# Performance work log

Measured on AMD Instinct MI355X. Metric: run time of the kernel, lower is better.

## Reference

```python
import jax, jax.numpy as jnp
import numpy as np

D_MODEL = 1024
NUM_HEADS = 16
HEAD_DIM = D_MODEL // NUM_HEADS
D_FF = 4096
B, S = 4, 2048
EPS = 1e-5


def layernorm(x, gamma, beta):
    mu = jnp.mean(x, axis=-1, keepdims=True)
    var = jnp.mean(jnp.square(x - mu), axis=-1, keepdims=True)
    return (x - mu) * jax.lax.rsqrt(var + EPS) * gamma + beta


def setup_inputs() -> dict:
    key = jax.random.key(0)
    ks = jax.random.split(key, 16)
    s_in = 1.0 / np.sqrt(D_MODEL)
    s_ff = 1.0 / np.sqrt(D_FF)
    return {
        "x": jax.random.normal(ks[0], (B, S, D_MODEL), jnp.float32),
        "Wq": jax.random.normal(ks[1], (D_MODEL, D_MODEL), jnp.float32) * s_in,
        "bq": jnp.zeros((D_MODEL,), jnp.float32),
        "Wk": jax.random.normal(ks[2], (D_MODEL, D_MODEL), jnp.float32) * s_in,
        "bk": jnp.zeros((D_MODEL,), jnp.float32),
        "Wv": jax.random.normal(ks[3], (D_MODEL, D_MODEL), jnp.float32) * s_in,
        "bv": jnp.zeros((D_MODEL,), jnp.float32),
        "Wo": jax.random.normal(ks[4], (D_MODEL, D_MODEL), jnp.float32) * s_in,
        "bo": jnp.zeros((D_MODEL,), jnp.float32),
        "W1": jax.random.normal(ks[5], (D_MODEL, D_FF), jnp.float32) * s_in,
        "b1": jnp.zeros((D_FF,), jnp.float32),
        "W2": jax.random.normal(ks[6], (D_FF, D_MODEL), jnp.float32) * s_ff,
        "b2": jnp.zeros((D_MODEL,), jnp.float32),
        "g1": jnp.ones((D_MODEL,), jnp.float32),
        "be1": jnp.zeros((D_MODEL,), jnp.float32),
        "g2": jnp.ones((D_MODEL,), jnp.float32),
        "be2": jnp.zeros((D_MODEL,), jnp.float32),
    }


def reference(x, Wq, bq, Wk, bk, Wv, bv, Wo, bo, W1, b1, W2, b2, g1, be1, g2, be2):
    # multi-head self-attention (dropout is identity at eval)
    def split_heads(t):  # [B,S,D] -> [B,H,S,hd]
        return t.reshape(B, S, NUM_HEADS, HEAD_DIM).transpose(0, 2, 1, 3)

    q = split_heads(x @ Wq + bq)
    k = split_heads(x @ Wk + bk)
    v = split_heads(x @ Wv + bv)
    scores = jnp.einsum("bhqd,bhkd->bhqk", q, k) / np.sqrt(HEAD_DIM)
    attn = jax.nn.softmax(scores, axis=-1)
    out = jnp.einsum("bhqk,bhkd->bhqd", attn, v)
    out = out.transpose(0, 2, 1, 3).reshape(B, S, D_MODEL)
    attn_out = out @ Wo + bo

    h = layernorm(x + attn_out, g1, be1)
    ff = jax.nn.relu(h @ W1 + b1) @ W2 + b2
    return layernorm(h + ff, g2, be2)
```

## Files before the change

kernel.cpp:

```cpp
#include <hip/hip_runtime.h>
#include <hip/hip_bf16.h>


#define DM    1024
#define DFF   4096
#define NH    16
#define HD    64
#define BATCH 4
#define SEQ   2048
#define TOK   (BATCH * SEQ)

typedef __attribute__((ext_vector_type(8))) __bf16 bf16x8;
typedef __attribute__((ext_vector_type(4))) float f32x4;
typedef __attribute__((ext_vector_type(16))) float f32x16;
typedef __attribute__((ext_vector_type(4))) unsigned short u16x4;

typedef const __attribute__((address_space(1))) unsigned int* gas1_t;
typedef __attribute__((address_space(3))) unsigned int* las3_t;

__device__ __forceinline__ void gl_lds16(const void* g, void* l) {
  __builtin_amdgcn_global_load_lds((gas1_t)g, (las3_t)l, 16, 0, 0);
}

__device__ __forceinline__ unsigned short f2bu(float x) {
  return __builtin_bit_cast(unsigned short, __float2bfloat16(x));
}

__device__ __forceinline__ unsigned pk_bf16_trunc(float hi, float lo) {
  return __builtin_amdgcn_perm(__builtin_bit_cast(unsigned, hi),
                               __builtin_bit_cast(unsigned, lo), 0x07060302u);
}

__global__ __launch_bounds__(256) void cast_bf16(
    const float* __restrict__ in, unsigned short* __restrict__ out, int n4) {
  int i = blockIdx.x * 256 + threadIdx.x;
  if (i >= n4) return;
  float4 v = ((const float4*)in)[i];
  u16x4 o = {f2bu(v.x), f2bu(v.y), f2bu(v.z), f2bu(v.w)};
  ((u16x4*)out)[i] = o;
}

__global__ __launch_bounds__(256) void transpose_cast(
    const float* __restrict__ in, unsigned short* __restrict__ out, int K, int N) {
  __shared__ float tile[32][33];
  int n0 = blockIdx.x * 32, k0 = blockIdx.y * 32;
  int tx = threadIdx.x, ty = threadIdx.y;
#pragma unroll
  for (int i = 0; i < 4; ++i)
    tile[ty + 8 * i][tx] = in[(size_t)(k0 + ty + 8 * i) * N + n0 + tx];
  __syncthreads();
#pragma unroll
  for (int i = 0; i < 4; ++i)
    out[(size_t)(n0 + ty + 8 * i) * K + k0 + tx] = f2bu(tile[tx][ty + 8 * i]);
}

__global__ __launch_bounds__(256) void transpose_cast4(
    const float* __restrict__ A0, const float* __restrict__ A1,
    const float* __restrict__ A2, const float* __restrict__ A3,
    unsigned short* __restrict__ O0, unsigned short* __restrict__ O1,
    unsigned short* __restrict__ O2, unsigned short* __restrict__ O3) {
  __shared__ float tile[32][33];
  const float* in; unsigned short* out;
  switch (blockIdx.z) {
    case 0: in = A0; out = O0; break;
    case 1: in = A1; out = O1; break;
    case 2: in = A2; out = O2; break;
    default: in = A3; out = O3; break;
  }
  int n0 = blockIdx.x * 32, k0 = blockIdx.y * 32;
  int tx = threadIdx.x, ty = threadIdx.y;
#pragma unroll
  for (int i = 0; i < 4; ++i)
    tile[ty + 8 * i][tx] = in[(size_t)(k0 + ty + 8 * i) * DM + n0 + tx];
  __syncthreads();
#pragma unroll
  for (int i = 0; i < 4; ++i)
    out[(size_t)(n0 + ty + 8 * i) * DM + k0 + tx] = f2bu(tile[tx][ty + 8 * i]);
}

__device__ __forceinline__ void gemm_mainloop(
    const unsigned short* __restrict__ A, const unsigned short* __restrict__ Bt,
    int K, int m0, int n0, unsigned short* As, unsigned short* Bs,
    f32x16 acc[2][2]) {
  const int tid = threadIdx.x, lane = tid & 63, w = tid >> 6;
  const int l31 = lane & 31, khalf = lane >> 5;
  const int wr = w >> 1, wc = w & 1;
  const int rk = (l31 >> 1) & 3;

  const unsigned short* ag[2];
  const unsigned short* bg[2];
  char* ldsA[2]; char* ldsB[2];
#pragma unroll
  for (int i = 0; i < 2; ++i) {
    int f = (i * 4 + w) * 64 + lane;
    int row = f >> 2;
    int col = ((f & 3) ^ ((row >> 1) & 3)) * 8;
    ag[i] = A + (size_t)(m0 + row) * K + col;
    bg[i] = Bt + (size_t)(n0 + row) * K + col;
    ldsA[i] = (char*)As + (size_t)((i * 4 + w) * 1024);
    ldsB[i] = (char*)Bs + (size_t)((i * 4 + w) * 1024);
  }

  for (int kb = 0; kb < K; kb += 32) {
#pragma unroll
    for (int i = 0; i < 2; ++i) {
      gl_lds16(ag[i], ldsA[i]);
      gl_lds16(bg[i], ldsB[i]);
      ag[i] += 32;
      bg[i] += 32;
    }
    __syncthreads();
#pragma unroll
    for (int kk = 0; kk < 2; ++kk) {
      const int sw = ((kk * 2 + khalf) ^ rk) * 16;
      bf16x8 aF[2], bF[2];
#pragma unroll
      for (int t = 0; t < 2; ++t) {
        aF[t] = *(const bf16x8*)((const char*)As + (wr * 64 + t * 32 + l31) * 64 + sw);
        bF[t] = *(const bf16x8*)((const char*)Bs + (wc * 64 + t * 32 + l31) * 64 + sw);
      }
#pragma unroll
      for (int mi = 0; mi < 2; ++mi)
#pragma unroll
        for (int ni = 0; ni < 2; ++ni)
          acc[mi][ni] = __builtin_amdgcn_mfma_f32_32x32x16_bf16(
              aF[mi], bF[ni], acc[mi][ni], 0, 0, 0);
    }
    __syncthreads();
  }
}


__global__ __launch_bounds__(256) void gemm_bt(
    const unsigned short* __restrict__ A, const unsigned short* __restrict__ Bt,
    const float* __restrict__ bias, void* __restrict__ Cout,
    int N, int K, float alpha, int relu, int ofp32) {
  __shared__ unsigned short As[128 * 32];
  __shared__ unsigned short Bs[128 * 32];
  const int tid = threadIdx.x, lane = tid & 63, w = tid >> 6;
  const int l31 = lane & 31, khalf = lane >> 5;
  const int m0 = blockIdx.y * 128, n0 = blockIdx.x * 128;
  const int wr = w >> 1, wc = w & 1;

  f32x16 acc[2][2];
#pragma unroll
  for (int mi = 0; mi < 2; ++mi)
#pragma unroll
    for (int ni = 0; ni < 2; ++ni)
#pragma unroll
      for (int r = 0; r < 16; ++r) acc[mi][ni][r] = 0.f;

  gemm_mainloop(A, Bt, K, m0, n0, As, Bs, acc);

#pragma unroll
  for (int ni = 0; ni < 2; ++ni) {
    int col = n0 + wc * 64 + ni * 32 + l31;
    float bvv = bias[col];
#pragma unroll
    for (int mi = 0; mi < 2; ++mi) {
#pragma unroll
      for (int g = 0; g < 4; ++g) {
        int rbase = m0 + wr * 64 + mi * 32 + g * 8 + khalf * 4;
#pragma unroll
        for (int r = 0; r < 4; ++r) {
          float val = alpha * (acc[mi][ni][g * 4 + r] + bvv);
          if (relu) val = fmaxf(val, 0.f);
          size_t idx = (size_t)(rbase + r) * N + col;
          if (ofp32) ((float*)Cout)[idx] = val;
          else ((unsigned short*)Cout)[idx] = f2bu(val);
        }
      }
    }
  }
}

#define QSCALE 0.18033688f

__global__ __launch_bounds__(256) void gemm_qkv(
    const unsigned short* __restrict__ A, const unsigned short* __restrict__ Bt,
    const float* __restrict__ bq, const float* __restrict__ bk,
    const float* __restrict__ bv,
    unsigned short* __restrict__ Qb, unsigned short* __restrict__ Kb,
    unsigned short* __restrict__ Vtg) {
  __shared__ unsigned short As[128 * 32];
  __shared__ unsigned short Bs[128 * 32];
  const int tid = threadIdx.x, lane = tid & 63, w = tid >> 6;
  const int l31 = lane & 31, khalf = lane >> 5;
  const int m0 = blockIdx.y * 128, n0 = blockIdx.x * 128;
  const int wr = w >> 1, wc = w & 1;

  f32x16 acc[2][2];
#pragma unroll
  for (int mi = 0; mi < 2; ++mi)
#pragma unroll
    for (int ni = 0; ni < 2; ++ni)
#pragma unroll
      for (int r = 0; r < 16; ++r) acc[mi][ni][r] = 0.f;

  gemm_mainloop(A, Bt, DM, m0, n0, As, Bs, acc);

  const int region = n0 >> 10;
  const int nloc0 = (n0 & 1023) + wc * 64;
  if (region < 2) {
    unsigned short* Out = region ? Kb : Qb;
    const float* bias = region ? bk : bq;
    const float alpha = region ? 1.0f : QSCALE;
#pragma unroll
    for (int ni = 0; ni < 2; ++ni) {
      int col = nloc0 + ni * 32 + l31;
      float bvv = bias[col];
#pragma unroll
      for (int mi = 0; mi < 2; ++mi) {
#pragma unroll
        for (int g = 0; g < 4; ++g) {
          int rbase = m0 + wr * 64 + mi * 32 + g * 8 + khalf * 4;
#pragma unroll
          for (int r = 0; r < 4; ++r)
            Out[(size_t)(rbase + r) * DM + col] =
                f2bu(alpha * (acc[mi][ni][g * 4 + r] + bvv));
        }
      }
    }
  } else {
#pragma unroll
    for (int ni = 0; ni < 2; ++ni) {
      int col = nloc0 + ni * 32 + l31;
      float bvv = bv[col];
      int hh = col >> 6, dl = col & 63;
#pragma unroll
      for (int mi = 0; mi < 2; ++mi) {
#pragma unroll
        for (int g = 0; g < 4; ++g) {
          int sbase = m0 + wr * 64 + mi * 32 + g * 8 + khalf * 4;
          int b_ = sbase >> 11, s0 = sbase & 2047;
          u16x4 pk;
#pragma unroll
          for (int r = 0; r < 4; ++r) pk[r] = f2bu(acc[mi][ni][g * 4 + r] + bvv);
          *(u16x4*)(Vtg + ((size_t)((b_ * NH + hh) * HD + dl)) * SEQ + s0) = pk;
        }
      }
    }
  }
}

__global__ __launch_bounds__(256) void attn_kernel(
    const unsigned short* __restrict__ Q, const unsigned short* __restrict__ K,
    const unsigned short* __restrict__ Vtg, unsigned short* __restrict__ O) {
  __shared__ unsigned short Kt[2][64 * 64];
  __shared__ unsigned short Vt[2][64 * 64];
  __shared__ unsigned short Pt[4][32 * 64];
  __shared__ __align__(16) float redL[4][32];

  const int tid = threadIdx.x, lane = tid & 63, w = tid >> 6;
  const int l15 = lane & 15, quad = lane >> 4;
  const int q0 = blockIdx.x * 128;
  const int bh = blockIdx.y, b = bh >> 4, hh = bh & 15;
  const size_t tokbase = (size_t)b * SEQ;

  bf16x8 qf[2][2];
#pragma unroll
  for (int qg = 0; qg < 2; ++qg)
#pragma unroll
    for (int kk = 0; kk < 2; ++kk)
      qf[qg][kk] = *(const bf16x8*)(Q +
          (tokbase + q0 + w * 32 + qg * 16 + l15) * DM + hh * HD + kk * 32 + quad * 8);

  float l_run[2] = {0.f, 0.f};
  f32x4 Oacc[2][4];
#pragma unroll
  for (int qg = 0; qg < 2; ++qg)
#pragma unroll
    for (int nt = 0; nt < 4; ++nt) Oacc[qg][nt] = {0.f, 0.f, 0.f, 0.f};

  char* ptw = (char*)&Pt[w][0];

  int rowS[2], csrcS[2];
#pragma unroll
  for (int i = 0; i < 2; ++i) {
    int f = (i * 4 + w) * 64 + lane;
    rowS[i] = f >> 3;
    csrcS[i] = ((f & 7) ^ (rowS[i] & 7)) * 8;
  }
  const unsigned short* kg[2];
  const unsigned short* vg[2];
  char* ldsK[2][2]; char* ldsV[2][2];
#pragma unroll
  for (int i = 0; i < 2; ++i) {
    kg[i] = K + (tokbase + rowS[i]) * DM + hh * HD + csrcS[i];
    vg[i] = Vtg + ((size_t)bh * HD + rowS[i]) * SEQ + csrcS[i];
#pragma unroll
    for (int bb = 0; bb < 2; ++bb) {
      ldsK[bb][i] = (char*)Kt[bb] + (size_t)((i * 4 + w) * 1024);
      ldsV[bb][i] = (char*)Vt[bb] + (size_t)((i * 4 + w) * 1024);
    }
  }

#pragma unroll
  for (int i = 0; i < 2; ++i) {
    gl_lds16(kg[i], ldsK[0][i]);
    gl_lds16(vg[i], ldsV[0][i]);
    kg[i] += 64 * DM;
    vg[i] += 64;
  }

  for (int j = 0; j < SEQ / 64; ++j) {
    const int buf = j & 1;
    __syncthreads();
    if (j + 1 < SEQ / 64) {
#pragma unroll
      for (int i = 0; i < 2; ++i) {
        gl_lds16(kg[i], ldsK[buf ^ 1][i]);
        gl_lds16(vg[i], ldsV[buf ^ 1][i]);
        kg[i] += 64 * DM;
        vg[i] += 64;
      }
    }

    const char* ktb = (const char*)Kt[buf];
    const char* vtb = (const char*)Vt[buf];

    f32x4 S[2][4];
#pragma unroll
    for (int qg = 0; qg < 2; ++qg)
#pragma unroll
      for (int mt = 0; mt < 4; ++mt) S[qg][mt] = {0.f, 0.f, 0.f, 0.f};
#pragma unroll
    for (int kk = 0; kk < 2; ++kk) {
#pragma unroll
      for (int mt = 0; mt < 4; ++mt) {
        bf16x8 aK = *(const bf16x8*)(ktb + (mt * 16 + l15) * 128 +
                                     (((kk * 4 + quad) ^ (l15 & 7)) * 16));
        S[0][mt] = __builtin_amdgcn_mfma_f32_16x16x32_bf16(aK, qf[0][kk], S[0][mt], 0, 0, 0);
        S[1][mt] = __builtin_amdgcn_mfma_f32_16x16x32_bf16(aK, qf[1][kk], S[1][mt], 0, 0, 0);
      }
    }

#pragma unroll
    for (int qg = 0; qg < 2; ++qg) {
      float rs = 0.f;
#pragma unroll
      for (int mt = 0; mt < 4; ++mt) {
        float p0 = __builtin_amdgcn_exp2f(S[qg][mt][0]);
        float p1 = __builtin_amdgcn_exp2f(S[qg][mt][1]);
        float p2 = __builtin_amdgcn_exp2f(S[qg][mt][2]);
        float p3 = __builtin_amdgcn_exp2f(S[qg][mt][3]);
        rs += (p0 + p1) + (p2 + p3);
        uint2 pk = {pk_bf16_trunc(p1, p0), pk_bf16_trunc(p3, p2)};
        *(uint2*)(ptw + (qg * 16 + l15) * 128 +
                  (((mt * 2 + (quad >> 1)) ^ (l15 & 7)) * 16 + (quad & 1) * 8)) = pk;
      }
      l_run[qg] += rs;
    }

#pragma unroll
    for (int kk = 0; kk < 2; ++kk) {
      bf16x8 aP[2];
#pragma unroll
      for (int qg = 0; qg < 2; ++qg)
        aP[qg] = *(const bf16x8*)(ptw + (qg * 16 + l15) * 128 +
                                  (((kk * 4 + quad) ^ (l15 & 7)) * 16));
#pragma unroll
      for (int nt = 0; nt < 4; ++nt) {
        bf16x8 bV = *(const bf16x8*)(vtb + (nt * 16 + l15) * 128 +
                                     (((kk * 4 + quad) ^ (l15 & 7)) * 16));
        Oacc[0][nt] = __builtin_amdgcn_mfma_f32_16x16x32_bf16(aP[0], bV, Oacc[0][nt], 0, 0, 0);
        Oacc[1][nt] = __builtin_amdgcn_mfma_f32_16x16x32_bf16(aP[1], bV, Oacc[1][nt], 0, 0, 0);
      }
    }
  }

#pragma unroll
  for (int qg = 0; qg < 2; ++qg) {
    l_run[qg] += __shfl_xor(l_run[qg], 16);
    l_run[qg] += __shfl_xor(l_run[qg], 32);
    if (lane < 16) redL[w][qg * 16 + l15] = l_run[qg];
  }
#pragma unroll
  for (int qg = 0; qg < 2; ++qg) {
    f32x4 lv = *(const f32x4*)&redL[w][qg * 16 + quad * 4];
    f32x4 li;
#pragma unroll
    for (int r = 0; r < 4; ++r) li[r] = 1.0f / lv[r];
#pragma unroll
    for (int nt = 0; nt < 4; ++nt)
#pragma unroll
      for (int r = 0; r < 4; ++r) {
        size_t tok = tokbase + q0 + w * 32 + qg * 16 + quad * 4 + r;
        O[tok * DM + hh * HD + nt * 16 + l15] = f2bu(Oacc[qg][nt][r] * li[r]);
      }
  }
}

__global__ __launch_bounds__(256) void ln_res(
    const float* __restrict__ base, const float* __restrict__ delta,
    const float* __restrict__ gamma, const float* __restrict__ beta,
    float* __restrict__ outf, unsigned short* __restrict__ outb) {
  __shared__ float red[8];
  const int row = blockIdx.x, tid = threadIdx.x;
  const size_t rb = (size_t)row * DM;
  float4 xv = ((const float4*)(base + rb))[tid];
  float4 dv = ((const float4*)(delta + rb))[tid];
  float s0 = xv.x + dv.x, s1 = xv.y + dv.y, s2 = xv.z + dv.z, s3 = xv.w + dv.w;
  float t = s0 + s1 + s2 + s3;
#pragma unroll
  for (int m = 1; m < 64; m <<= 1) t += __shfl_xor(t, m);
  if ((tid & 63) == 0) red[tid >> 6] = t;
  __syncthreads();
  float mu = (red[0] + red[1] + red[2] + red[3]) * (1.0f / DM);
  float d0 = s0 - mu, d1 = s1 - mu, d2 = s2 - mu, d3 = s3 - mu;
  float v = d0 * d0 + d1 * d1 + d2 * d2 + d3 * d3;
#pragma unroll
  for (int m = 1; m < 64; m <<= 1) v += __shfl_xor(v, m);
  if ((tid & 63) == 0) red[4 + (tid >> 6)] = v;
  __syncthreads();
  float var = (red[4] + red[5] + red[6] + red[7]) * (1.0f / DM);
  float rs = rsqrtf(var + 1e-5f);
  float4 gv = ((const float4*)gamma)[tid];
  float4 bv = ((const float4*)beta)[tid];
  float o0 = d0 * rs * gv.x + bv.x;
  float o1 = d1 * rs * gv.y + bv.y;
  float o2 = d2 * rs * gv.z + bv.z;
  float o3 = d3 * rs * gv.w + bv.w;
  float4 ov = {o0, o1, o2, o3};
  ((float4*)(outf + rb))[tid] = ov;
  if (outb) {
    u16x4 ob = {f2bu(o0), f2bu(o1), f2bu(o2), f2bu(o3)};
    ((u16x4*)(outb + rb))[tid] = ob;
  }
}

extern "C" void kernel_launch(void* const* d_in, const int* in_sizes, int n_in,
                              void* d_out, int out_size, void* d_ws, size_t ws_size,
                              hipStream_t stream) {
  const float* x   = (const float*)d_in[0];
  const float* Wq  = (const float*)d_in[1];  const float* bq  = (const float*)d_in[2];
  const float* Wk  = (const float*)d_in[3];  const float* bk  = (const float*)d_in[4];
  const float* Wv  = (const float*)d_in[5];  const float* bvv = (const float*)d_in[6];
  const float* Wo  = (const float*)d_in[7];  const float* bo  = (const float*)d_in[8];
  const float* W1  = (const float*)d_in[9];  const float* b1  = (const float*)d_in[10];
  const float* W2  = (const float*)d_in[11]; const float* b2  = (const float*)d_in[12];
  const float* g1  = (const float*)d_in[13]; const float* be1 = (const float*)d_in[14];
  const float* g2  = (const float*)d_in[15]; const float* be2 = (const float*)d_in[16];

  char* ws = (char*)d_ws;
  const size_t MB = 1ull << 20;
  unsigned short* xb    = (unsigned short*)(ws + 0 * MB);
  unsigned short* wqkvT = (unsigned short*)(ws + 16 * MB);
  unsigned short* woT   = (unsigned short*)(ws + 22 * MB);
  unsigned short* w1T   = (unsigned short*)(ws + 24 * MB);
  unsigned short* w2T   = (unsigned short*)(ws + 32 * MB);
  unsigned short* Qb    = (unsigned short*)(ws + 40 * MB);
  unsigned short* Kb    = (unsigned short*)(ws + 56 * MB);
  unsigned short* Vtg   = (unsigned short*)(ws + 72 * MB);
  unsigned short* aO    = (unsigned short*)(ws + 104 * MB);
  float*          prj   = (float*)(ws + 120 * MB);
  float*          h     = (float*)(ws + 152 * MB);
  unsigned short* hb    = (unsigned short*)(ws + 0 * MB);
  unsigned short* ffm   = (unsigned short*)(ws + 40 * MB);
  float*          ffo   = (float*)(ws + 104 * MB);
  (void)ws_size; (void)in_sizes; (void)n_in; (void)out_size;

  cast_bf16<<<TOK * DM / 4 / 256, 256, 0, stream>>>(x, xb, TOK * DM / 4);
  transpose_cast4<<<dim3(DM / 32, DM / 32, 4), dim3(32, 8), 0, stream>>>(
      Wq, Wk, Wv, Wo, wqkvT, wqkvT + 1024 * 1024, wqkvT + 2048 * 1024, woT);
  transpose_cast<<<dim3(DFF / 32, DM / 32), dim3(32, 8), 0, stream>>>(W1, w1T, DM, DFF);
  transpose_cast<<<dim3(DM / 32, DFF / 32), dim3(32, 8), 0, stream>>>(W2, w2T, DFF, DM);

  gemm_qkv<<<dim3(3 * DM / 128, TOK / 128), 256, 0, stream>>>(
      xb, wqkvT, bq, bk, bvv, Qb, Kb, Vtg);

  attn_kernel<<<dim3(SEQ / 128, BATCH * NH), 256, 0, stream>>>(Qb, Kb, Vtg, aO);

  gemm_bt<<<dim3(DM / 128, TOK / 128), 256, 0, stream>>>(aO, woT, bo, prj, DM, DM, 1.0f, 0, 1);
  ln_res<<<TOK, 256, 0, stream>>>(x, prj, g1, be1, h, hb);

  gemm_bt<<<dim3(DFF / 128, TOK / 128), 256, 0, stream>>>(hb, w1T, b1, ffm, DFF, DM, 1.0f, 1, 0);
  gemm_bt<<<dim3(DM / 128, TOK / 128), 256, 0, stream>>>(ffm, w2T, b2, ffo, DM, DFF, 1.0f, 0, 1);

  ln_res<<<TOK, 256, 0, stream>>>(h, ffo, g2, be2, (float*)d_out, nullptr);
}
```

Baseline: 604.2 us.

## Switch GEMMs to 256x256 tiles with double-buffered pipelined mainloop and split-K FFN2

Replaces the 128x128 single-buffer GEMM mainloop with a 256x256-tile, 512-thread kernel. It uses K=64 double-buffered LDS staging, issues loads in quarters interleaved with MFMA phases via explicit vmcnt waits and barriers, and raises MFMA priority with setprio. The FFN down-projection is split into two K halves written to separate fp32 buffers, and the final layernorm sums both partials. This aims to raise arithmetic intensity and overlap global loads with compute, at the cost of more LDS and registers per block and fewer blocks for the 1024-wide GEMMs.

```diff
diff --git a/kernel.cpp b/kernel.cpp
--- a/kernel.cpp
+++ b/kernel.cpp
@@ -78,167 +78,222 @@
     out[(size_t)(n0 + ty + 8 * i) * DM + k0 + tx] = f2bu(tile[tx][ty + 8 * i]);
 }
 
-__device__ __forceinline__ void gemm_mainloop(
-    const unsigned short* __restrict__ A, const unsigned short* __restrict__ Bt,
-    int K, int m0, int n0, unsigned short* As, unsigned short* Bs,
-    f32x16 acc[2][2]) {
+template <int QM, int QN>
+__device__ __forceinline__ void phase_mma(
+    const unsigned short* As, const unsigned short* Bs, int bufofs,
+    int wr, int wc, int l31, int khalf, f32x16 acc[2][2][2]) {
+  const char* Ah = (const char*)(As + bufofs + QM * 8192);
+  const char* Bh = (const char*)(Bs + bufofs + QN * 8192);
+  const int rA0 = wr * 64 + l31, rA1 = rA0 + 32, rB = wc * 32 + l31;
+  bf16x8 a0[4], a1[4], bb[4];
+#pragma unroll
+  for (int ks = 0; ks < 4; ++ks) {
+    const int c = ks * 2 + khalf;
+    a0[ks] = *(const bf16x8*)(Ah + rA0 * 128 + ((c ^ (rA0 & 7)) << 4));
+    a1[ks] = *(const bf16x8*)(Ah + rA1 * 128 + ((c ^ (rA1 & 7)) << 4));
+    bb[ks] = *(const bf16x8*)(Bh + rB * 128 + ((c ^ (rB & 7)) << 4));
+  }
+  __builtin_amdgcn_s_setprio(1);
+#pragma unroll
+  for (int ks = 0; ks < 4; ++ks) {
+    acc[QM][QN][0] = __builtin_amdgcn_mfma_f32_32x32x16_bf16(
+        a0[ks], bb[ks], acc[QM][QN][0], 0, 0, 0);
+    acc[QM][QN][1] = __builtin_amdgcn_mfma_f32_32x32x16_bf16(
+        a1[ks], bb[ks], acc[QM][QN][1], 0, 0, 0);
+  }
+  __builtin_amdgcn_s_setprio(0);
+}
+
+__device__ __forceinline__ void mainloop256(
+    const unsigned short* __restrict__ A, int lda,
+    const unsigned short* __restrict__ Bt, int ldb, int Kl,
+    int m0, int n0, unsigned short* As, unsigned short* Bs,
+    f32x16 acc[2][2][2]) {
   const int tid = threadIdx.x, lane = tid & 63, w = tid >> 6;
   const int l31 = lane & 31, khalf = lane >> 5;
-  const int wr = w >> 1, wc = w & 1;
-  const int rk = (l31 >> 1) & 3;
-
-  const unsigned short* ag[2];
-  const unsigned short* bg[2];
-  char* ldsA[2]; char* ldsB[2];
-#pragma unroll
-  for (int i = 0; i < 2; ++i) {
-    int f = (i * 4 + w) * 64 + lane;
-    int row = f >> 2;
-    int col = ((f & 3) ^ ((row >> 1) & 3)) * 8;
-    ag[i] = A + (size_t)(m0 + row) * K + col;
-    bg[i] = Bt + (size_t)(n0 + row) * K + col;
-    ldsA[i] = (char*)As + (size_t)((i * 4 + w) * 1024);
-    ldsB[i] = (char*)Bs + (size_t)((i * 4 + w) * 1024);
-  }
-
-  for (int kb = 0; kb < K; kb += 32) {
+  const int wr = w >> 2, wc = w & 3;
+
+  const unsigned short* pa[2][2];
+  const unsigned short* pb[2][2];
+#pragma unroll
+  for (int h = 0; h < 2; ++h)
 #pragma unroll
     for (int i = 0; i < 2; ++i) {
-      gl_lds16(ag[i], ldsA[i]);
-      gl_lds16(bg[i], ldsB[i]);
-      ag[i] += 32;
-      bg[i] += 32;
-    }
-    __syncthreads();
-#pragma unroll
-    for (int kk = 0; kk < 2; ++kk) {
-      const int sw = ((kk * 2 + khalf) ^ rk) * 16;
-      bf16x8 aF[2], bF[2];
-#pragma unroll
-      for (int t = 0; t < 2; ++t) {
-        aF[t] = *(const bf16x8*)((const char*)As + (wr * 64 + t * 32 + l31) * 64 + sw);
-        bF[t] = *(const bf16x8*)((const char*)Bs + (wc * 64 + t * 32 + l31) * 64 + sw);
-      }
-#pragma unroll
-      for (int mi = 0; mi < 2; ++mi)
-#pragma unroll
-        for (int ni = 0; ni < 2; ++ni)
-          acc[mi][ni] = __builtin_amdgcn_mfma_f32_32x32x16_bf16(
-              aF[mi], bF[ni], acc[mi][ni], 0, 0, 0);
-    }
-    __syncthreads();
-  }
-}
-
-
-__global__ __launch_bounds__(256) void gemm_bt(
-    const unsigned short* __restrict__ A, const unsigned short* __restrict__ Bt,
-    const float* __restrict__ bias, void* __restrict__ Cout,
-    int N, int K, float alpha, int relu, int ofp32) {
-  __shared__ unsigned short As[128 * 32];
-  __shared__ unsigned short Bs[128 * 32];
+      const int g = (i * 8 + w) * 64 + lane;
+      const int r = g >> 3;
+      const int cs = ((g & 7) ^ (r & 7)) * 8;
+      pa[h][i] = A + (size_t)(m0 + h * 128 + r) * lda + cs;
+      pb[h][i] = Bt + (size_t)(n0 + h * 128 + r) * ldb + cs;
+    }
+  const int wofs = w * 512;
+
+#define STA(BUF, H, I) gl_lds16(pa[H][I], As + (BUF) * 16384 + (H) * 8192 + (I) * 4096 + wofs)
+#define STB(BUF, H, I) gl_lds16(pb[H][I], Bs + (BUF) * 16384 + (H) * 8192 + (I) * 4096 + wofs)
+#define ADV_A(H) { pa[H][0] += 64; pa[H][1] += 64; }
+#define ADV_B(H) { pb[H][0] += 64; pb[H][1] += 64; }
+
+  STA(0, 0, 0); STA(0, 0, 1); ADV_A(0);
+  STB(0, 0, 0); STB(0, 0, 1); ADV_B(0);
+  STB(0, 1, 0); STB(0, 1, 1); ADV_B(1);
+  STA(0, 1, 0); STA(0, 1, 1); ADV_A(1);
+
+#define PH(BUF, QMv, QNv, WAITSTR, STG)                                  \
+  asm volatile(WAITSTR ::: "memory");                                    \
+  STG;                                                                   \
+  phase_mma<QMv, QNv>(As, Bs, (BUF) * 16384, wr, wc, l31, khalf, acc)
+
+#define TILE_STEADY(B)                                                        \
+  PH(B, 0, 0, "s_waitcnt vmcnt(4)\n\ts_barrier",                              \
+     { STA(B ^ 1, 0, 0); STA(B ^ 1, 0, 1); ADV_A(0); });                      \
+  PH(B, 0, 1, "s_waitcnt vmcnt(4)\n\ts_barrier",                              \
+     { STB(B ^ 1, 0, 0); STB(B ^ 1, 0, 1); ADV_B(0); });                      \
+  PH(B, 1, 0, "s_waitcnt vmcnt(4)\n\ts_barrier",                              \
+     { STB(B ^ 1, 1, 0); STB(B ^ 1, 1, 1); ADV_B(1); });                      \
+  PH(B, 1, 1, "s_barrier",                                                    \
+     { STA(B ^ 1, 1, 0); STA(B ^ 1, 1, 1); ADV_A(1); })
+
+  const int NT = Kl >> 6;
+  for (int t = 0; t + 2 < NT; t += 2) {
+    TILE_STEADY(0);
+    TILE_STEADY(1);
+  }
+  TILE_STEADY(0);
+  PH(1, 0, 0, "s_waitcnt vmcnt(4)\n\ts_barrier", {});
+  PH(1, 0, 1, "s_waitcnt vmcnt(2)\n\ts_barrier", {});
+  PH(1, 1, 0, "s_waitcnt vmcnt(0)\n\ts_barrier", {});
+  PH(1, 1, 1, "s_barrier", {});
+
+#undef TILE_STEADY
+#undef PH
+#undef ADV_B
+#undef ADV_A
+#undef STB
+#undef STA
+}
+
+
+__global__ __launch_bounds__(512, 2) void gemm256(
+    const unsigned short* __restrict__ A, int lda,
+    const unsigned short* __restrict__ Bt, int ldb, int Kl,
+    const float* __restrict__ bias, void* __restrict__ C0,
+    void* __restrict__ C1, int N, float alpha, int relu, int ofp32) {
+  __shared__ unsigned short As[32768];
+  __shared__ unsigned short Bs[32768];
   const int tid = threadIdx.x, lane = tid & 63, w = tid >> 6;
   const int l31 = lane & 31, khalf = lane >> 5;
-  const int m0 = blockIdx.y * 128, n0 = blockIdx.x * 128;
-  const int wr = w >> 1, wc = w & 1;
-
-  f32x16 acc[2][2];
-#pragma unroll
-  for (int mi = 0; mi < 2; ++mi)
-#pragma unroll
-    for (int ni = 0; ni < 2; ++ni)
-#pragma unroll
-      for (int r = 0; r < 16; ++r) acc[mi][ni][r] = 0.f;
-
-  gemm_mainloop(A, Bt, K, m0, n0, As, Bs, acc);
-
-#pragma unroll
-  for (int ni = 0; ni < 2; ++ni) {
-    int col = n0 + wc * 64 + ni * 32 + l31;
-    float bvv = bias[col];
-#pragma unroll
-    for (int mi = 0; mi < 2; ++mi) {
-#pragma unroll
-      for (int g = 0; g < 4; ++g) {
-        int rbase = m0 + wr * 64 + mi * 32 + g * 8 + khalf * 4;
-#pragma unroll
-        for (int r = 0; r < 4; ++r) {
-          float val = alpha * (acc[mi][ni][g * 4 + r] + bvv);
-          if (relu) val = fmaxf(val, 0.f);
-          size_t idx = (size_t)(rbase + r) * N + col;
-          if (ofp32) ((float*)Cout)[idx] = val;
-          else ((unsigned short*)Cout)[idx] = f2bu(val);
+  const int wr = w >> 2, wc = w & 3;
+  const int m0 = blockIdx.y * 256, n0 = blockIdx.x * 256;
+  const int koff = blockIdx.z * Kl;
+  void* Cout = blockIdx.z ? C1 : C0;
+  const float* be = blockIdx.z ? nullptr : bias;
+
+  f32x16 acc[2][2][2];
+#pragma unroll
+  for (int qm = 0; qm < 2; ++qm)
+#pragma unroll
+    for (int qn = 0; qn < 2; ++qn)
+#pragma unroll
+      for (int mi = 0; mi < 2; ++mi)
+#pragma unroll
+        for (int r = 0; r < 16; ++r) acc[qm][qn][mi][r] = 0.f;
+
+  mainloop256(A + koff, lda, Bt + koff, ldb, Kl, m0, n0, As, Bs, acc);
+
+#pragma unroll
+  for (int qn = 0; qn < 2; ++qn) {
+    const int col = n0 + qn * 128 + wc * 32 + l31;
+    const float bvv = be ? be[col] : 0.f;
+#pragma unroll
+    for (int qm = 0; qm < 2; ++qm)
+#pragma unroll
+      for (int mi = 0; mi < 2; ++mi) {
+#pragma unroll
+        for (int g = 0; g < 4; ++g) {
+          const int rbase = m0 + qm * 128 + wr * 64 + mi * 32 + g * 8 + khalf * 4;
+#pragma unroll
+          for (int r = 0; r < 4; ++r) {
+            float val = alpha * (acc[qm][qn][mi][g * 4 + r] + bvv);
+            if (relu) val = fmaxf(val, 0.f);
+            size_t idx = (size_t)(rbase + r) * N + col;
+            if (ofp32) ((float*)Cout)[idx] = val;
+            else ((unsigned short*)Cout)[idx] = f2bu(val);
+          }
         }
       }
-    }
   }
 }
 
 #define QSCALE 0.18033688f
 
-__global__ __launch_bounds__(256) void gemm_qkv(
+__global__ __launch_bounds__(512, 2) void gemm_qkv256(
     const unsigned short* __restrict__ A, const unsigned short* __restrict__ Bt,
     const float* __restrict__ bq, const float* __restrict__ bk,
     const float* __restrict__ bv,
     unsigned short* __restrict__ Qb, unsigned short* __restrict__ Kb,
     unsigned short* __restrict__ Vtg) {
-  __shared__ unsigned short As[128 * 32];
-  __shared__ unsigned short Bs[128 * 32];
+  __shared__ unsigned short As[32768];
+  __shared__ unsigned short Bs[32768];
   const int tid = threadIdx.x, lane = tid & 63, w = tid >> 6;
   const int l31 = lane & 31, khalf = lane >> 5;
-  const int m0 = blockIdx.y * 128, n0 = blockIdx.x * 128;
-  const int wr = w >> 1, wc = w & 1;
-
-  f32x16 acc[2][2];
-#pragma unroll
-  for (int mi = 0; mi < 2; ++mi)
-#pragma unroll
-    for (int ni = 0; ni < 2; ++ni)
-#pragma unroll
-      for (int r = 0; r < 16; ++r) acc[mi][ni][r] = 0.f;
-
-  gemm_mainloop(A, Bt, DM, m0, n0, As, Bs, acc);
+  const int wr = w >> 2, wc = w & 3;
+  const int m0 = blockIdx.y * 256, n0 = blockIdx.x * 256;
+
+  f32x16 acc[2][2][2];
+#pragma unroll
+  for (int qm = 0; qm < 2; ++qm)
+#pragma unroll
+    for (int qn = 0; qn < 2; ++qn)
+#pragma unroll
+      for (int mi = 0; mi < 2; ++mi)
+#pragma unroll
+        for (int r = 0; r < 16; ++r) acc[qm][qn][mi][r] = 0.f;
+
+  mainloop256(A, DM, Bt, DM, DM, m0, n0, As, Bs, acc);
 
   const int region = n0 >> 10;
-  const int nloc0 = (n0 & 1023) + wc * 64;
   if (region < 2) {
     unsigned short* Out = region ? Kb : Qb;
     const float* bias = region ? bk : bq;
     const float alpha = region ? 1.0f : QSCALE;
 #pragma unroll
-    for (int ni = 0; ni < 2; ++ni) {
-      int col = nloc0 + ni * 32 + l31;
-      float bvv = bias[col];
-#pragma unroll
-      for (int mi = 0; mi < 2; ++mi) {
-#pragma unroll
-        for (int g = 0; g < 4; ++g) {
-          int rbase = m0 + wr * 64 + mi * 32 + g * 8 + khalf * 4;
-#pragma unroll
-          for (int r = 0; r < 4; ++r)
-            Out[(size_t)(rbase + r) * DM + col] =
-                f2bu(alpha * (acc[mi][ni][g * 4 + r] + bvv));
+    for (int qn = 0; qn < 2; ++qn) {
+      const int col = (n0 & 1023) + qn * 128 + wc * 32 + l31;
+      const float bvv = bias[col];
+#pragma unroll
+      for (int qm = 0; qm < 2; ++qm)
+#pragma unroll
+        for (int mi = 0; mi < 2; ++mi) {
+#pragma unroll
+          for (int g = 0; g < 4; ++g) {
+            const int rbase = m0 + qm * 128 + wr * 64 + mi * 32 + g * 8 + khalf * 4;
+#pragma unroll
+            for (int r = 0; r < 4; ++r)
+              Out[(size_t)(rbase + r) * DM + col] =
+                  f2bu(alpha * (acc[qm][qn][mi][g * 4 + r] + bvv));
+          }
         }
-      }
     }
   } else {
 #pragma unroll
-    for (int ni = 0; ni < 2; ++ni) {
-      int col = nloc0 + ni * 32 + l31;
-      float bvv = bv[col];
-      int hh = col >> 6, dl = col & 63;
-#pragma unroll
-      for (int mi = 0; mi < 2; ++mi) {
-#pragma unroll
-        for (int g = 0; g < 4; ++g) {
-          int sbase = m0 + wr * 64 + mi * 32 + g * 8 + khalf * 4;
-          int b_ = sbase >> 11, s0 = sbase & 2047;
-          u16x4 pk;
-#pragma unroll
-          for (int r = 0; r < 4; ++r) pk[r] = f2bu(acc[mi][ni][g * 4 + r] + bvv);
-          *(u16x4*)(Vtg + ((size_t)((b_ * NH + hh) * HD + dl)) * SEQ + s0) = pk;
+    for (int qn = 0; qn < 2; ++qn) {
+      const int col = (n0 & 1023) + qn * 128 + wc * 32 + l31;
+      const float bvv = bv[col];
+      const int hh = col >> 6, dl = col & 63;
+#pragma unroll
+      for (int qm = 0; qm < 2; ++qm)
+#pragma unroll
+        for (int mi = 0; mi < 2; ++mi) {
+#pragma unroll
+          for (int g = 0; g < 4; ++g) {
+            const int sbase = m0 + qm * 128 + wr * 64 + mi * 32 + g * 8 + khalf * 4;
+            const int b_ = sbase >> 11, s0 = sbase & 2047;
+            u16x4 pk;
+#pragma unroll
+            for (int r = 0; r < 4; ++r)
+              pk[r] = f2bu(acc[qm][qn][mi][g * 4 + r] + bvv);
+            *(u16x4*)(Vtg + ((size_t)((b_ * NH + hh) * HD + dl)) * SEQ + s0) = pk;
+          }
         }
-      }
     }
   }
 }
@@ -392,23 +447,28 @@
 }
 
 __global__ __launch_bounds__(256) void ln_res(
-    const float* __restrict__ base, const float* __restrict__ delta,
+    const float* __restrict__ base, const float* __restrict__ d0,
+    const float* __restrict__ d1,
     const float* __restrict__ gamma, const float* __restrict__ beta,
     float* __restrict__ outf, unsigned short* __restrict__ outb) {
   __shared__ float red[8];
   const int row = blockIdx.x, tid = threadIdx.x;
   const size_t rb = (size_t)row * DM;
   float4 xv = ((const float4*)(base + rb))[tid];
-  float4 dv = ((const float4*)(delta + rb))[tid];
+  float4 dv = ((const float4*)(d0 + rb))[tid];
   float s0 = xv.x + dv.x, s1 = xv.y + dv.y, s2 = xv.z + dv.z, s3 = xv.w + dv.w;
+  if (d1) {
+    float4 ev = ((const float4*)(d1 + rb))[tid];
+    s0 += ev.x; s1 += ev.y; s2 += ev.z; s3 += ev.w;
+  }
   float t = s0 + s1 + s2 + s3;
 #pragma unroll
   for (int m = 1; m < 64; m <<= 1) t += __shfl_xor(t, m);
   if ((tid & 63) == 0) red[tid >> 6] = t;
   __syncthreads();
   float mu = (red[0] + red[1] + red[2] + red[3]) * (1.0f / DM);
-  float d0 = s0 - mu, d1 = s1 - mu, d2 = s2 - mu, d3 = s3 - mu;
-  float v = d0 * d0 + d1 * d1 + d2 * d2 + d3 * d3;
+  float dd0 = s0 - mu, dd1 = s1 - mu, dd2 = s2 - mu, dd3 = s3 - mu;
+  float v = dd0 * dd0 + dd1 * dd1 + dd2 * dd2 + dd3 * dd3;
 #pragma unroll
   for (int m = 1; m < 64; m <<= 1) v += __shfl_xor(v, m);
   if ((tid & 63) == 0) red[4 + (tid >> 6)] = v;
@@ -417,10 +477,10 @@
   float rs = rsqrtf(var + 1e-5f);
   float4 gv = ((const float4*)gamma)[tid];
   float4 bv = ((const float4*)beta)[tid];
-  float o0 = d0 * rs * gv.x + bv.x;
-  float o1 = d1 * rs * gv.y + bv.y;
-  float o2 = d2 * rs * gv.z + bv.z;
-  float o3 = d3 * rs * gv.w + bv.w;
+  float o0 = dd0 * rs * gv.x + bv.x;
+  float o1 = dd1 * rs * gv.y + bv.y;
+  float o2 = dd2 * rs * gv.z + bv.z;
+  float o3 = dd3 * rs * gv.w + bv.w;
   float4 ov = {o0, o1, o2, o3};
   ((float4*)(outf + rb))[tid] = ov;
   if (outb) {
@@ -458,6 +518,7 @@
   unsigned short* hb    = (unsigned short*)(ws + 0 * MB);
   unsigned short* ffm   = (unsigned short*)(ws + 40 * MB);
   float*          ffo   = (float*)(ws + 104 * MB);
+  float*          ffo2  = (float*)(ws + 0 * MB);
   (void)ws_size; (void)in_sizes; (void)n_in; (void)out_size;
 
   cast_bf16<<<TOK * DM / 4 / 256, 256, 0, stream>>>(x, xb, TOK * DM / 4);
@@ -466,16 +527,19 @@
   transpose_cast<<<dim3(DFF / 32, DM / 32), dim3(32, 8), 0, stream>>>(W1, w1T, DM, DFF);
   transpose_cast<<<dim3(DM / 32, DFF / 32), dim3(32, 8), 0, stream>>>(W2, w2T, DFF, DM);
 
-  gemm_qkv<<<dim3(3 * DM / 128, TOK / 128), 256, 0, stream>>>(
+  gemm_qkv256<<<dim3(3 * DM / 256, TOK / 256), 512, 0, stream>>>(
       xb, wqkvT, bq, bk, bvv, Qb, Kb, Vtg);
 
   attn_kernel<<<dim3(SEQ / 128, BATCH * NH), 256, 0, stream>>>(Qb, Kb, Vtg, aO);
 
-  gemm_bt<<<dim3(DM / 128, TOK / 128), 256, 0, stream>>>(aO, woT, bo, prj, DM, DM, 1.0f, 0, 1);
-  ln_res<<<TOK, 256, 0, stream>>>(x, prj, g1, be1, h, hb);
-
-  gemm_bt<<<dim3(DFF / 128, TOK / 128), 256, 0, stream>>>(hb, w1T, b1, ffm, DFF, DM, 1.0f, 1, 0);
-  gemm_bt<<<dim3(DM / 128, TOK / 128), 256, 0, stream>>>(ffm, w2T, b2, ffo, DM, DFF, 1.0f, 0, 1);
-
-  ln_res<<<TOK, 256, 0, stream>>>(h, ffo, g2, be2, (float*)d_out, nullptr);
-}
+  gemm256<<<dim3(DM / 256, TOK / 256, 1), 512, 0, stream>>>(
+      aO, DM, woT, DM, DM, bo, prj, nullptr, DM, 1.0f, 0, 1);
+  ln_res<<<TOK, 256, 0, stream>>>(x, prj, nullptr, g1, be1, h, hb);
+
+  gemm256<<<dim3(DFF / 256, TOK / 256, 1), 512, 0, stream>>>(
+      hb, DM, w1T, DM, DM, b1, ffm, nullptr, DFF, 1.0f, 1, 0);
+  gemm256<<<dim3(DM / 256, TOK / 256, 2), 512, 0, stream>>>(
+      ffm, DFF, w2T, DFF, DFF / 2, b2, ffo, ffo2, DM, 1.0f, 0, 1);
+
+  ln_res<<<TOK, 256, 0, stream>>>(h, ffo, ffo2, g2, be2, (float*)d_out, nullptr);
+}
```

Result: slower. 639.7 us (+5.9%).

## Switch GEMMs to 16x16x32 MFMA tiles with XCD-aware block remapping

Applied to the files above, without the earlier changes.

Rewrites the shared GEMM main loop to use 4x4 tiles of 16x16x32 bf16 MFMAs per wave instead of 2x2 tiles of 32x32x16. It also drops the XOR LDS swizzle in favour of a plain layout, since the new fragment reads are contiguous. A block-index remap spreads neighbouring tiles across the XCDs to improve L2 locality, and separate lda/ldb/K arguments are added. ln_res gains an optional second residual input, but every call passes null, so it only prepares for later work such as split-K.

```diff
diff --git a/kernel.cpp b/kernel.cpp
--- a/kernel.cpp
+++ b/kernel.cpp
@@ -12,7 +12,6 @@
 
 typedef __attribute__((ext_vector_type(8))) __bf16 bf16x8;
 typedef __attribute__((ext_vector_type(4))) float f32x4;
-typedef __attribute__((ext_vector_type(16))) float f32x16;
 typedef __attribute__((ext_vector_type(4))) unsigned short u16x4;
 
 typedef const __attribute__((address_space(1))) unsigned int* gas1_t;
@@ -78,97 +77,99 @@
     out[(size_t)(n0 + ty + 8 * i) * DM + k0 + tx] = f2bu(tile[tx][ty + 8 * i]);
 }
 
-__device__ __forceinline__ void gemm_mainloop(
-    const unsigned short* __restrict__ A, const unsigned short* __restrict__ Bt,
-    int K, int m0, int n0, unsigned short* As, unsigned short* Bs,
-    f32x16 acc[2][2]) {
+__device__ __forceinline__ void mainloop128(
+    const unsigned short* __restrict__ A, int lda,
+    const unsigned short* __restrict__ Bt, int ldb, int Kl,
+    int m0, int n0, unsigned short* As, unsigned short* Bs,
+    f32x4 acc[4][4]) {
   const int tid = threadIdx.x, lane = tid & 63, w = tid >> 6;
-  const int l31 = lane & 31, khalf = lane >> 5;
+  const int l15 = lane & 15, quad = lane >> 4;
   const int wr = w >> 1, wc = w & 1;
-  const int rk = (l31 >> 1) & 3;
-
-  const unsigned short* ag[2];
-  const unsigned short* bg[2];
-  char* ldsA[2]; char* ldsB[2];
+
+  const unsigned short* pa[2];
+  const unsigned short* pb[2];
 #pragma unroll
   for (int i = 0; i < 2; ++i) {
-    int f = (i * 4 + w) * 64 + lane;
-    int row = f >> 2;
-    int col = ((f & 3) ^ ((row >> 1) & 3)) * 8;
-    ag[i] = A + (size_t)(m0 + row) * K + col;
-    bg[i] = Bt + (size_t)(n0 + row) * K + col;
-    ldsA[i] = (char*)As + (size_t)((i * 4 + w) * 1024);
-    ldsB[i] = (char*)Bs + (size_t)((i * 4 + w) * 1024);
-  }
-
-  for (int kb = 0; kb < K; kb += 32) {
+    const int g = i * 256 + tid;
+    const int row = g >> 2, ch = (g & 3) * 8;
+    pa[i] = A + (size_t)(m0 + row) * lda + ch;
+    pb[i] = Bt + (size_t)(n0 + row) * ldb + ch;
+  }
+
+  for (int kb = 0; kb < Kl; kb += 32) {
 #pragma unroll
     for (int i = 0; i < 2; ++i) {
-      gl_lds16(ag[i], ldsA[i]);
-      gl_lds16(bg[i], ldsB[i]);
-      ag[i] += 32;
-      bg[i] += 32;
+      gl_lds16(pa[i], (char*)As + i * 4096 + w * 1024);
+      gl_lds16(pb[i], (char*)Bs + i * 4096 + w * 1024);
+      pa[i] += 32;
+      pb[i] += 32;
     }
     __syncthreads();
-#pragma unroll
-    for (int kk = 0; kk < 2; ++kk) {
-      const int sw = ((kk * 2 + khalf) ^ rk) * 16;
-      bf16x8 aF[2], bF[2];
-#pragma unroll
-      for (int t = 0; t < 2; ++t) {
-        aF[t] = *(const bf16x8*)((const char*)As + (wr * 64 + t * 32 + l31) * 64 + sw);
-        bF[t] = *(const bf16x8*)((const char*)Bs + (wc * 64 + t * 32 + l31) * 64 + sw);
-      }
-#pragma unroll
-      for (int mi = 0; mi < 2; ++mi)
-#pragma unroll
-        for (int ni = 0; ni < 2; ++ni)
-          acc[mi][ni] = __builtin_amdgcn_mfma_f32_32x32x16_bf16(
-              aF[mi], bF[ni], acc[mi][ni], 0, 0, 0);
-    }
+
+    bf16x8 aF[4], bF[4];
+#pragma unroll
+    for (int m = 0; m < 4; ++m)
+      aF[m] = *(const bf16x8*)((const char*)As +
+                               (wr * 64 + m * 16 + l15) * 64 + quad * 16);
+#pragma unroll
+    for (int n = 0; n < 4; ++n)
+      bF[n] = *(const bf16x8*)((const char*)Bs +
+                               (wc * 64 + n * 16 + l15) * 64 + quad * 16);
+#pragma unroll
+    for (int m = 0; m < 4; ++m)
+#pragma unroll
+      for (int n = 0; n < 4; ++n)
+        acc[m][n] = __builtin_amdgcn_mfma_f32_16x16x32_bf16(
+            aF[m], bF[n], acc[m][n], 0, 0, 0);
     __syncthreads();
   }
 }
 
 
-__global__ __launch_bounds__(256) void gemm_bt(
-    const unsigned short* __restrict__ A, const unsigned short* __restrict__ Bt,
+__device__ __forceinline__ void xcd_swizzle(int& bx, int& by) {
+  const int gx = gridDim.x, nxy = gx * gridDim.y;
+  int lin = by * gx + bx;
+  lin = (lin & 7) * (nxy >> 3) + (lin >> 3);
+  bx = lin % gx;
+  by = lin / gx;
+}
+
+__global__ __launch_bounds__(256) void gemm128(
+    const unsigned short* __restrict__ A, int lda,
+    const unsigned short* __restrict__ Bt, int ldb, int Kl,
     const float* __restrict__ bias, void* __restrict__ Cout,
-    int N, int K, float alpha, int relu, int ofp32) {
+    int N, float alpha, int relu, int ofp32) {
   __shared__ unsigned short As[128 * 32];
   __shared__ unsigned short Bs[128 * 32];
   const int tid = threadIdx.x, lane = tid & 63, w = tid >> 6;
-  const int l31 = lane & 31, khalf = lane >> 5;
-  const int m0 = blockIdx.y * 128, n0 = blockIdx.x * 128;
+  const int l15 = lane & 15, quad = lane >> 4;
   const int wr = w >> 1, wc = w & 1;
-
-  f32x16 acc[2][2];
-#pragma unroll
-  for (int mi = 0; mi < 2; ++mi)
-#pragma unroll
-    for (int ni = 0; ni < 2; ++ni)
-#pragma unroll
-      for (int r = 0; r < 16; ++r) acc[mi][ni][r] = 0.f;
-
-  gemm_mainloop(A, Bt, K, m0, n0, As, Bs, acc);
-
-#pragma unroll
-  for (int ni = 0; ni < 2; ++ni) {
-    int col = n0 + wc * 64 + ni * 32 + l31;
-    float bvv = bias[col];
-#pragma unroll
-    for (int mi = 0; mi < 2; ++mi) {
-#pragma unroll
-      for (int g = 0; g < 4; ++g) {
-        int rbase = m0 + wr * 64 + mi * 32 + g * 8 + khalf * 4;
-#pragma unroll
-        for (int r = 0; r < 4; ++r) {
-          float val = alpha * (acc[mi][ni][g * 4 + r] + bvv);
-          if (relu) val = fmaxf(val, 0.f);
-          size_t idx = (size_t)(rbase + r) * N + col;
-          if (ofp32) ((float*)Cout)[idx] = val;
-          else ((unsigned short*)Cout)[idx] = f2bu(val);
-        }
+  int bx = blockIdx.x, by = blockIdx.y;
+  xcd_swizzle(bx, by);
+  const int m0 = by * 128, n0 = bx * 128;
+
+  f32x4 acc[4][4];
+#pragma unroll
+  for (int m = 0; m < 4; ++m)
+#pragma unroll
+    for (int n = 0; n < 4; ++n) acc[m][n] = {0.f, 0.f, 0.f, 0.f};
+
+  mainloop128(A, lda, Bt, ldb, Kl, m0, n0, As, Bs, acc);
+
+#pragma unroll
+  for (int n = 0; n < 4; ++n) {
+    const int col = n0 + wc * 64 + n * 16 + l15;
+    const float bvv = bias[col];
+#pragma unroll
+    for (int m = 0; m < 4; ++m) {
+      const int rbase = m0 + wr * 64 + m * 16 + quad * 4;
+#pragma unroll
+      for (int r = 0; r < 4; ++r) {
+        float val = alpha * (acc[m][n][r] + bvv);
+        if (relu) val = fmaxf(val, 0.f);
+        size_t idx = (size_t)(rbase + r) * N + col;
+        if (ofp32) ((float*)Cout)[idx] = val;
+        else ((unsigned short*)Cout)[idx] = f2bu(val);
       }
     }
   }
@@ -176,7 +177,7 @@
 
 #define QSCALE 0.18033688f
 
-__global__ __launch_bounds__(256) void gemm_qkv(
+__global__ __launch_bounds__(256) void gemm_qkv128(
     const unsigned short* __restrict__ A, const unsigned short* __restrict__ Bt,
     const float* __restrict__ bq, const float* __restrict__ bk,
     const float* __restrict__ bv,
@@ -185,59 +186,52 @@
   __shared__ unsigned short As[128 * 32];
   __shared__ unsigned short Bs[128 * 32];
   const int tid = threadIdx.x, lane = tid & 63, w = tid >> 6;
-  const int l31 = lane & 31, khalf = lane >> 5;
-  const int m0 = blockIdx.y * 128, n0 = blockIdx.x * 128;
+  const int l15 = lane & 15, quad = lane >> 4;
   const int wr = w >> 1, wc = w & 1;
-
-  f32x16 acc[2][2];
-#pragma unroll
-  for (int mi = 0; mi < 2; ++mi)
-#pragma unroll
-    for (int ni = 0; ni < 2; ++ni)
-#pragma unroll
-      for (int r = 0; r < 16; ++r) acc[mi][ni][r] = 0.f;
-
-  gemm_mainloop(A, Bt, DM, m0, n0, As, Bs, acc);
+  int bx = blockIdx.x, by = blockIdx.y;
+  xcd_swizzle(bx, by);
+  const int m0 = by * 128, n0 = bx * 128;
+
+  f32x4 acc[4][4];
+#pragma unroll
+  for (int m = 0; m < 4; ++m)
+#pragma unroll
+    for (int n = 0; n < 4; ++n) acc[m][n] = {0.f, 0.f, 0.f, 0.f};
+
+  mainloop128(A, DM, Bt, DM, DM, m0, n0, As, Bs, acc);
 
   const int region = n0 >> 10;
-  const int nloc0 = (n0 & 1023) + wc * 64;
   if (region < 2) {
     unsigned short* Out = region ? Kb : Qb;
     const float* bias = region ? bk : bq;
     const float alpha = region ? 1.0f : QSCALE;
 #pragma unroll
-    for (int ni = 0; ni < 2; ++ni) {
-      int col = nloc0 + ni * 32 + l31;
-      float bvv = bias[col];
-#pragma unroll
-      for (int mi = 0; mi < 2; ++mi) {
-#pragma unroll
-        for (int g = 0; g < 4; ++g) {
-          int rbase = m0 + wr * 64 + mi * 32 + g * 8 + khalf * 4;
-#pragma unroll
-          for (int r = 0; r < 4; ++r)
-            Out[(size_t)(rbase + r) * DM + col] =
-                f2bu(alpha * (acc[mi][ni][g * 4 + r] + bvv));
-        }
+    for (int n = 0; n < 4; ++n) {
+      const int col = (n0 & 1023) + wc * 64 + n * 16 + l15;
+      const float bvv = bias[col];
+#pragma unroll
+      for (int m = 0; m < 4; ++m) {
+        const int rbase = m0 + wr * 64 + m * 16 + quad * 4;
+#pragma unroll
+        for (int r = 0; r < 4; ++r)
+          Out[(size_t)(rbase + r) * DM + col] =
+              f2bu(alpha * (acc[m][n][r] + bvv));
       }
     }
   } else {
 #pragma unroll
-    for (int ni = 0; ni < 2; ++ni) {
-      int col = nloc0 + ni * 32 + l31;
-      float bvv = bv[col];
-      int hh = col >> 6, dl = col & 63;
-#pragma unroll
-      for (int mi = 0; mi < 2; ++mi) {
-#pragma unroll
-        for (int g = 0; g < 4; ++g) {
-          int sbase = m0 + wr * 64 + mi * 32 + g * 8 + khalf * 4;
-          int b_ = sbase >> 11, s0 = sbase & 2047;
-          u16x4 pk;
-#pragma unroll
-          for (int r = 0; r < 4; ++r) pk[r] = f2bu(acc[mi][ni][g * 4 + r] + bvv);
-          *(u16x4*)(Vtg + ((size_t)((b_ * NH + hh) * HD + dl)) * SEQ + s0) = pk;
-        }
+    for (int n = 0; n < 4; ++n) {
+      const int col = (n0 & 1023) + wc * 64 + n * 16 + l15;
+      const float bvv = bv[col];
+      const int hh = col >> 6, dl = col & 63;
+#pragma unroll
+      for (int m = 0; m < 4; ++m) {
+        const int sbase = m0 + wr * 64 + m * 16 + quad * 4;
+        const int b_ = sbase >> 11, s0 = sbase & 2047;
+        u16x4 pk;
+#pragma unroll
+        for (int r = 0; r < 4; ++r) pk[r] = f2bu(acc[m][n][r] + bvv);
+        *(u16x4*)(Vtg + ((size_t)((b_ * NH + hh) * HD + dl)) * SEQ + s0) = pk;
       }
     }
   }
@@ -392,23 +386,28 @@
 }
 
 __global__ __launch_bounds__(256) void ln_res(
-    const float* __restrict__ base, const float* __restrict__ delta,
+    const float* __restrict__ base, const float* __restrict__ d0,
+    const float* __restrict__ d1,
     const float* __restrict__ gamma, const float* __restrict__ beta,
     float* __restrict__ outf, unsigned short* __restrict__ outb) {
   __shared__ float red[8];
   const int row = blockIdx.x, tid = threadIdx.x;
   const size_t rb = (size_t)row * DM;
   float4 xv = ((const float4*)(base + rb))[tid];
-  float4 dv = ((const float4*)(delta + rb))[tid];
+  float4 dv = ((const float4*)(d0 + rb))[tid];
   float s0 = xv.x + dv.x, s1 = xv.y + dv.y, s2 = xv.z + dv.z, s3 = xv.w + dv.w;
+  if (d1) {
+    float4 ev = ((const float4*)(d1 + rb))[tid];
+    s0 += ev.x; s1 += ev.y; s2 += ev.z; s3 += ev.w;
+  }
   float t = s0 + s1 + s2 + s3;
 #pragma unroll
   for (int m = 1; m < 64; m <<= 1) t += __shfl_xor(t, m);
   if ((tid & 63) == 0) red[tid >> 6] = t;
   __syncthreads();
   float mu = (red[0] + red[1] + red[2] + red[3]) * (1.0f / DM);
-  float d0 = s0 - mu, d1 = s1 - mu, d2 = s2 - mu, d3 = s3 - mu;
-  float v = d0 * d0 + d1 * d1 + d2 * d2 + d3 * d3;
+  float dd0 = s0 - mu, dd1 = s1 - mu, dd2 = s2 - mu, dd3 = s3 - mu;
+  float v = dd0 * dd0 + dd1 * dd1 + dd2 * dd2 + dd3 * dd3;
 #pragma unroll
   for (int m = 1; m < 64; m <<= 1) v += __shfl_xor(v, m);
   if ((tid & 63) == 0) red[4 + (tid >> 6)] = v;
@@ -417,10 +416,10 @@
   float rs = rsqrtf(var + 1e-5f);
   float4 gv = ((const float4*)gamma)[tid];
   float4 bv = ((const float4*)beta)[tid];
-  float o0 = d0 * rs * gv.x + bv.x;
-  float o1 = d1 * rs * gv.y + bv.y;
-  float o2 = d2 * rs * gv.z + bv.z;
-  float o3 = d3 * rs * gv.w + bv.w;
+  float o0 = dd0 * rs * gv.x + bv.x;
+  float o1 = dd1 * rs * gv.y + bv.y;
+  float o2 = dd2 * rs * gv.z + bv.z;
+  float o3 = dd3 * rs * gv.w + bv.w;
   float4 ov = {o0, o1, o2, o3};
   ((float4*)(outf + rb))[tid] = ov;
   if (outb) {
@@ -466,16 +465,19 @@
   transpose_cast<<<dim3(DFF / 32, DM / 32), dim3(32, 8), 0, stream>>>(W1, w1T, DM, DFF);
   transpose_cast<<<dim3(DM / 32, DFF / 32), dim3(32, 8), 0, stream>>>(W2, w2T, DFF, DM);
 
-  gemm_qkv<<<dim3(3 * DM / 128, TOK / 128), 256, 0, stream>>>(
+  gemm_qkv128<<<dim3(3 * DM / 128, TOK / 128), 256, 0, stream>>>(
       xb, wqkvT, bq, bk, bvv, Qb, Kb, Vtg);
 
   attn_kernel<<<dim3(SEQ / 128, BATCH * NH), 256, 0, stream>>>(Qb, Kb, Vtg, aO);
 
-  gemm_bt<<<dim3(DM / 128, TOK / 128), 256, 0, stream>>>(aO, woT, bo, prj, DM, DM, 1.0f, 0, 1);
-  ln_res<<<TOK, 256, 0, stream>>>(x, prj, g1, be1, h, hb);
-
-  gemm_bt<<<dim3(DFF / 128, TOK / 128), 256, 0, stream>>>(hb, w1T, b1, ffm, DFF, DM, 1.0f, 1, 0);
-  gemm_bt<<<dim3(DM / 128, TOK / 128), 256, 0, stream>>>(ffm, w2T, b2, ffo, DM, DFF, 1.0f, 0, 1);
-
-  ln_res<<<TOK, 256, 0, stream>>>(h, ffo, g2, be2, (float*)d_out, nullptr);
-}
+  gemm128<<<dim3(DM / 128, TOK / 128), 256, 0, stream>>>(
+      aO, DM, woT, DM, DM, bo, prj, DM, 1.0f, 0, 1);
+  ln_res<<<TOK, 256, 0, stream>>>(x, prj, nullptr, g1, be1, h, hb);
+
+  gemm128<<<dim3(DFF / 128, TOK / 128), 256, 0, stream>>>(
+      hb, DM, w1T, DM, DM, b1, ffm, DFF, 1.0f, 1, 0);
+  gemm128<<<dim3(DM / 128, TOK / 128), 256, 0, stream>>>(
+      ffm, DFF, w2T, DFF, DFF, b2, ffo, DM, 1.0f, 0, 1);
+
+  ln_res<<<TOK, 256, 0, stream>>>(h, ffo, nullptr, g2, be2, (float*)d_out, nullptr);
+}
```

After: 587.7 us. -2.7%, faster.
